# Kernel optimization log

Measured on AMD Instinct MI355X. Metric: run time of the kernel, lower is better.

## Reference

```python
import jax, jax.numpy as jnp
import numpy as np

B, D, H, L, E, NL, P, IMG, NT = 32, 768, 8, 6, 8, 256, 16, 224, 10
G = IMG // P          # 14 patches per side
NP = G * G            # 196 patches
HD = D // H           # 96 head dim
TOPK = 2
KEEP = 0.25
EPS = 1e-5


def layer_norm(x, g, b):
    m = x.mean(-1, keepdims=True)
    v = ((x - m) ** 2).mean(-1, keepdims=True)
    return (x - m) / jnp.sqrt(v + EPS) * g + b


def mha(q, kv, in_w, in_b, out_w, out_b):
    # torch nn.MultiheadAttention: packed in_proj (3D, D), out_proj (D, D)
    wq, wk, wv = in_w[:D], in_w[D:2 * D], in_w[2 * D:]
    bq, bk, bv = in_b[:D], in_b[D:2 * D], in_b[2 * D:]

    def heads(x, w, b):
        y = x @ w.T + b                               # (B, S, D)
        return y.reshape(x.shape[0], x.shape[1], H, HD).transpose(0, 2, 1, 3)

    Q = heads(q, wq, bq)
    K = heads(kv, wk, bk)
    V = heads(kv, wv, bv)
    scores = jnp.einsum('bhqd,bhkd->bhqk', Q, K) / np.sqrt(HD).astype(np.float32)
    attn = jax.nn.softmax(scores, axis=-1)
    o = jnp.einsum('bhqk,bhkd->bhqd', attn, V)
    o = o.transpose(0, 2, 1, 3).reshape(q.shape[0], q.shape[1], D)
    return o @ out_w.T + out_b


def moe(x, rw, rb, w1, b1, w2, b2):
    # top-2 routing; renormalize the top-k weights with a second softmax
    Bq, S, _ = x.shape
    T = Bq * S
    xt = x.reshape(T, D)
    probs = jax.nn.softmax(xt @ rw.T + rb, axis=-1)       # (T, E)
    tw, ti = jax.lax.top_k(probs, TOPK)                   # (T, K)
    tw = jax.nn.softmax(tw, axis=-1)
    # combine weights per expert: (T, E), >0 only for the chosen experts
    combine = (jax.nn.one_hot(ti, E, dtype=x.dtype) * tw[..., None]).sum(axis=1)
    out = jnp.zeros_like(xt)
    for e in range(E):  # fixed small expert count
        h = jax.nn.gelu(xt @ w1[e].T + b1[e], approximate=False)
        out = out + (h @ w2[e].T + b2[e]) * combine[:, e:e + 1]
    return out.reshape(Bq, S, D)


def _forward(images, type_ids, mask_noise, conv_w, conv_b, pos_emb, type_emb,
             latents, ca_in_w, ca_in_b, ca_out_w, ca_out_b, ca_ln_g, ca_ln_b,
             sa_in_w, sa_in_b, sa_out_w, sa_out_b, ln1_g, ln1_b,
             router_w, router_b, e_w1, e_b1, e_w2, e_b2, ln2_g, ln2_b):
    b = images.shape[0]
    # non-overlapping conv patch embed == unfold + matmul
    xp = images.reshape(b, 3, G, P, G, P).transpose(0, 2, 4, 1, 3, 5)
    xp = xp.reshape(b, NP, 3 * P * P)
    patches = xp @ conv_w.reshape(D, -1).T + conv_b        # (B, NP, D)
    patches = patches + pos_emb + type_emb[type_ids][:, None, :]
    # random masking: keep n_visible patches chosen by argsort of noise
    n_visible = int(NP * KEEP)
    order = jnp.argsort(mask_noise, axis=1)
    visible_indices = order[:, :n_visible]
    masked_indices = order[:, n_visible:]
    visible = jnp.take_along_axis(patches, visible_indices[:, :, None], axis=1)
    # cross attention from latents to visible patches
    lat = jnp.broadcast_to(latents, (b, NL, D))
    lat = layer_norm(lat + mha(lat, visible, ca_in_w, ca_in_b, ca_out_w, ca_out_b),
                     ca_ln_g, ca_ln_b)
    for l in range(L):
        a = mha(lat, lat, sa_in_w[l], sa_in_b[l], sa_out_w[l], sa_out_b[l])
        lat = layer_norm(lat + a, ln1_g[l], ln1_b[l])
        m = moe(lat, router_w[l], router_b[l], e_w1[l], e_b1[l], e_w2[l], e_b2[l])
        lat = layer_norm(lat + m, ln2_g[l], ln2_b[l])
    return lat, visible_indices, masked_indices


def setup_inputs() -> dict:
    key = jax.random.key(0)
    ks = jax.random.split(key, 16)
    r = lambda k, shape, s=0.02: jax.random.normal(k, shape, dtype=jnp.float32) * s
    z = lambda shape: jnp.zeros(shape, jnp.float32)
    o = lambda shape: jnp.ones(shape, jnp.float32)
    inp = {}
    inp['images'] = jax.random.normal(ks[0], (B, 3, IMG, IMG), dtype=jnp.float32)
    inp['type_ids'] = jax.random.randint(ks[1], (B,), 0, NT)
    inp['mask_noise'] = jax.random.uniform(ks[2], (B, NP), dtype=jnp.float32)
    inp['conv_w'] = r(ks[3], (D, 3, P, P))
    inp['conv_b'] = z((D,))
    inp['pos_emb'] = r(ks[4], (1, NP, D), 1.0)
    inp['type_emb'] = r(ks[5], (NT, D), 1.0)
    inp['latents'] = r(ks[6], (NL, D), 1.0)
    inp['ca_in_w'] = r(ks[7], (3 * D, D)); inp['ca_in_b'] = z((3 * D,))
    inp['ca_out_w'] = r(ks[8], (D, D)); inp['ca_out_b'] = z((D,))
    inp['ca_ln_g'] = o((D,)); inp['ca_ln_b'] = z((D,))
    inp['sa_in_w'] = r(ks[9], (L, 3 * D, D)); inp['sa_in_b'] = z((L, 3 * D))
    inp['sa_out_w'] = r(ks[10], (L, D, D)); inp['sa_out_b'] = z((L, D))
    inp['ln1_g'] = o((L, D)); inp['ln1_b'] = z((L, D))
    inp['router_w'] = r(ks[11], (L, E, D)); inp['router_b'] = z((L, E))
    inp['e_w1'] = r(ks[12], (L, E, 2 * D, D)); inp['e_b1'] = z((L, E, 2 * D))
    inp['e_w2'] = r(ks[13], (L, E, D, 2 * D)); inp['e_b2'] = z((L, E, D))
    inp['ln2_g'] = o((L, D)); inp['ln2_b'] = z((L, D))
    return inp


def reference(images, type_ids, mask_noise, conv_w, conv_b, pos_emb, type_emb,
              latents, ca_in_w, ca_in_b, ca_out_w, ca_out_b, ca_ln_g, ca_ln_b,
              sa_in_w, sa_in_b, sa_out_w, sa_out_b, ln1_g, ln1_b,
              router_w, router_b, e_w1, e_b1, e_w2, e_b2, ln2_g, ln2_b):
    return _forward(images, type_ids, mask_noise, conv_w, conv_b, pos_emb,
                    type_emb, latents, ca_in_w, ca_in_b, ca_out_w, ca_out_b,
                    ca_ln_g, ca_ln_b, sa_in_w, sa_in_b, sa_out_w, sa_out_b,
                    ln1_g, ln1_b, router_w, router_b, e_w1, e_b1, e_w2, e_b2,
                    ln2_g, ln2_b)
```

## Files before the change

### kernel.cpp

```cpp
#include <hip/hip_runtime.h>

typedef unsigned short u16;
typedef unsigned int u32;
typedef __attribute__((ext_vector_type(8))) u16 u16x8;
typedef __attribute__((ext_vector_type(8))) __bf16 bf16x8;
typedef __attribute__((ext_vector_type(4))) float f32x4;

#define DEV static __device__ __forceinline__

DEV float b2f(u16 u){ unsigned int i = ((unsigned int)u)<<16; float f; __builtin_memcpy(&f,&i,4); return f; }
DEV u16 f2b(float f){ unsigned int x; __builtin_memcpy(&x,&f,4); x = x + 0x7fffu + ((x>>16)&1u); return (u16)(x>>16); }

DEV void gll16(const u16* g, u16* l){
    __builtin_amdgcn_global_load_lds(
        (const __attribute__((address_space(1))) u32*)(const void*)g,
        (__attribute__((address_space(3))) u32*)(void*)l, 16, 0, 0);
}

template<bool F32>
DEV u16x8 ld8(const void* base, long off){
    if constexpr (F32){
        const float* p = (const float*)base + off;
        float4 a = *(const float4*)p;
        float4 b = *(const float4*)(p+4);
        u16x8 r;
        r[0]=f2b(a.x); r[1]=f2b(a.y); r[2]=f2b(a.z); r[3]=f2b(a.w);
        r[4]=f2b(b.x); r[5]=f2b(b.y); r[6]=f2b(b.z); r[7]=f2b(b.w);
        return r;
    } else {
        return *(const u16x8*)((const u16*)base + off);
    }
}
template<bool F32>
DEV const void* vadd(const void* p, long elems){
    if constexpr (F32) return (const void*)((const float*)p + elems);
    else               return (const void*)((const u16*)p + elems);
}

#define LAT_ELEMS 6291456
#define NVIS 49
#define NMASK 147
#define T_TOK 8192
#define MOE_CAP 17408
#define MOE_HALF 8704
#define KOFF 6291456L
#define VOFF 12582912L

__global__ __launch_bounds__(256) void wconv(const float* __restrict__ src, u16* __restrict__ dst, long n)
{
    long i = ((long)blockIdx.x*256 + threadIdx.x)*8;
    if (i >= n) return;
    *(u16x8*)(dst + i) = ld8<true>(src, i);
}

__global__ __launch_bounds__(256) void argsort_k(const float* __restrict__ noise,
                                                 int* __restrict__ order,
                                                 float* __restrict__ dout,
                                                 u16* __restrict__ zbuf)
{
    __shared__ float vals[196];
    __shared__ int ord[196];
    int b = blockIdx.x, tid = threadIdx.x;
    if (b == 0 && tid < 128) zbuf[tid] = 0;
    if (tid < 196) vals[tid] = noise[b*196 + tid];
    __syncthreads();
    if (tid < 196){
        float vi = vals[tid]; int rank = 0;
        for (int j=0;j<196;j++){ float vj = vals[j]; rank += (vj < vi) || (vj == vi && j < tid); }
        ord[rank] = tid;
    }
    __syncthreads();
    if (tid < 196){
        int v = ord[tid];
        order[b*196 + tid] = v;
        if (tid < NVIS) dout[LAT_ELEMS + b*NVIS + tid] = (float)v;
        else            dout[LAT_ELEMS + 32*NVIS + b*NMASK + (tid - NVIS)] = (float)v;
    }
}

__global__ __launch_bounds__(256) void patch_gather(const float* __restrict__ images,
                                                    const int* __restrict__ order,
                                                    u16* __restrict__ Ap)
{
    int i = blockIdx.x*256 + threadIdx.x;
    int t = i/48, kc = i - t*48;
    if (t >= 1664) return;
    if (t >= 1568){
        u16x8 z{};
        *(u16x8*)(Ap + (long)t*768 + kc*16)     = z;
        *(u16x8*)(Ap + (long)t*768 + kc*16 + 8) = z;
        return;
    }
    int b = t/49, vi = t - b*49;
    int p = order[b*196 + vi];
    int c = kc >> 4, py = kc & 15;
    int gy = p/14, gx = p - gy*14;
    const float* src = images + (((long)(b*3 + c)*224 + gy*16 + py)*224 + gx*16);
    u16x8 o0 = ld8<true>(src, 0);
    u16x8 o1 = ld8<true>(src, 8);
    *(u16x8*)(Ap + (long)t*768 + kc*16)     = o0;
    *(u16x8*)(Ap + (long)t*768 + kc*16 + 8) = o1;
}

__global__ __launch_bounds__(256) void add_pos_type(u16* __restrict__ vis,
                                                    const int* __restrict__ order,
                                                    const int* __restrict__ type_ids,
                                                    const float* __restrict__ pos,
                                                    const float* __restrict__ temb)
{
    int i = blockIdx.x*256 + threadIdx.x;
    int t = i/96, dc = (i - t*96)*8;
    if (t >= 1568) return;
    int b = t/49, vi = t - b*49;
    int p = order[b*196 + vi], tb = type_ids[b];
    u16x8 a = *(u16x8*)(vis + (long)t*768 + dc);
    const float* pp = pos  + (long)p*768 + dc;
    const float* tt = temb + (long)tb*768 + dc;
    float4 p0 = *(const float4*)pp, p1 = *(const float4*)(pp+4);
    float4 t0 = *(const float4*)tt, t1 = *(const float4*)(tt+4);
    u16x8 o;
    o[0]=f2b(b2f(a[0])+p0.x+t0.x); o[1]=f2b(b2f(a[1])+p0.y+t0.y);
    o[2]=f2b(b2f(a[2])+p0.z+t0.z); o[3]=f2b(b2f(a[3])+p0.w+t0.w);
    o[4]=f2b(b2f(a[4])+p1.x+t1.x); o[5]=f2b(b2f(a[5])+p1.y+t1.y);
    o[6]=f2b(b2f(a[6])+p1.z+t1.z); o[7]=f2b(b2f(a[7])+p1.w+t1.w);
    *(u16x8*)(vis + (long)t*768 + dc) = o;
}

template<int BK, bool BIAS, bool GELU, int GRP, bool AF32, bool BF32, bool SWZ, bool GLL>
__global__ __launch_bounds__(256,4) void gemm_nt(
    const void* __restrict__ A, const void* __restrict__ B, const float* __restrict__ bias,
    u16* __restrict__ C,
    int M, int N, int K, int lda, int ldb, int ldc,
    float scale, int ZLO, int NB,
    long sAh, long sAl, long sBh, long sBl, long sCh, long sCl,
    const int* __restrict__ aoff, const int* __restrict__ tos, const u16* __restrict__ zbuf,
    int row_base, long sBE, long sBiasE)
{
    int bx = blockIdx.x, by = blockIdx.y;
    if (SWZ){
        int nx = gridDim.x, ny = gridDim.y;
        int nwg = nx*ny;
        int flat = by*nx + bx;
        int q = nwg >> 3, r = nwg & 7;
        int xcd = flat & 7, idx = flat >> 3;
        int wg = (xcd < r ? xcd*(q+1) : r*(q+1) + (xcd - r)*q) + idx;
        bx = wg % nx; by = wg / nx;
    }
    int z = blockIdx.z; int zh = z / ZLO, zl = z - zh*ZLO;
    const void* Ab = vadd<AF32>(A, zh*sAh + zl*sAl);
    const void* Bb = vadd<BF32>(B, zh*sBh + zl*sBl);
    u16* Cb = C + zh*sCh + zl*sCl;
    const float* biasb = bias;
    int row0 = by*128, col0 = bx*128;
    int lim = 0;
    if (GRP == 1 || GRP == 2){
        lim = aoff[8];
        int g0 = row_base + row0;
        if (g0 >= lim) return;
        int e = 0;
        #pragma unroll
        for (int i=1;i<8;i++) if (g0 >= aoff[i]) e = i;
        Bb = vadd<BF32>(B, (long)e*sBE);
        if (BIAS) biasb = bias + (long)e*sBiasE;
    }
    constexpr int SP = GLL ? BK : BK + 8;
    __shared__ __align__(16) u16 As[128*SP];
    __shared__ __align__(16) u16 Bs[128*SP];
    int tid = threadIdx.x;
    int lane = tid & 63, wv = tid >> 6;
    int wr = (wv>>1)*64, wc = (wv&1)*64;
    f32x4 acc[4][4];
    #pragma unroll
    for (int m=0;m<4;m++){
        #pragma unroll
        for (int n=0;n<4;n++) acc[m][n] = f32x4{0.f,0.f,0.f,0.f};
    }
    constexpr int RPC = BK/8;
    constexpr int RPI = 64/RPC;
    constexpr int NJ  = 32/RPI;
    constexpr int PER = 128*RPC/256;
    int tA[4];
    if (GRP == 1){
        if (GLL){
            #pragma unroll
            for (int j=0;j<NJ;j++){
                int r = wv*32 + j*RPI + (lane/RPC);
                tA[j] = tos[row_base + row0 + r];
            }
        } else {
            #pragma unroll
            for (int j=0;j<PER && j<4;j++){
                int c = j*256 + tid;
                tA[j] = tos[row_base + row0 + c/RPC];
            }
        }
    }
    for (int k0=0; k0<K; k0+=BK){
        if constexpr (GLL){
            #pragma unroll
            for (int j=0;j<NJ;j++){
                int r  = wv*32 + j*RPI + (lane/RPC);
                int ch = lane % RPC;
                const u16* sa;
                if (GRP == 1){
                    int t = tA[j];
                    sa = (t >= 0) ? (const u16*)Ab + (long)t*lda + k0 + ch*8 : zbuf + ch*8;
                } else {
                    sa = (const u16*)Ab + (long)(row0+r)*lda + k0 + ch*8;
                }
                gll16(sa, As + (wv*32 + j*RPI)*BK);
                const u16* sb = (col0 + r < NB) ? (const u16*)Bb + (long)(col0+r)*ldb + k0 + ch*8
                                                : zbuf + ch*8;
                gll16(sb, Bs + (wv*32 + j*RPI)*BK);
            }
        } else {
            #pragma unroll
            for (int j=0;j<PER;j++){
                int c = j*256 + tid;
                int r = c / RPC, cc = (c - r*RPC)*8;
                u16x8 va{}, vb{};
                if (GRP == 1){
                    int t = tA[j];
                    if (t >= 0) va = ld8<AF32>(Ab, (long)t*lda + k0 + cc);
                } else {
                    va = ld8<AF32>(Ab, (long)(row0+r)*lda + k0 + cc);
                }
                if (col0 + r < NB) vb = ld8<BF32>(Bb, (long)(col0+r)*ldb + k0 + cc);
                *(u16x8*)(As + r*SP + cc) = va;
                *(u16x8*)(Bs + r*SP + cc) = vb;
            }
        }
        __syncthreads();
        #pragma unroll
        for (int kk=0; kk<BK/32; kk++){
            bf16x8 af[4], bg[4];
            #pragma unroll
            for (int m=0;m<4;m++)
                af[m] = *(const bf16x8*)(As + (wr + m*16 + (lane&15))*SP + kk*32 + (lane>>4)*8);
            #pragma unroll
            for (int n=0;n<4;n++)
                bg[n] = *(const bf16x8*)(Bs + (wc + n*16 + (lane&15))*SP + kk*32 + (lane>>4)*8);
            #pragma unroll
            for (int m=0;m<4;m++){
                #pragma unroll
                for (int n=0;n<4;n++)
                    acc[m][n] = __builtin_amdgcn_mfma_f32_16x16x32_bf16(af[m], bg[n], acc[m][n], 0,0,0);
            }
        }
        __syncthreads();
    }
    #pragma unroll
    for (int m=0;m<4;m++){
        int rbase = row0 + wr + m*16 + ((lane>>4)<<2);
        #pragma unroll
        for (int n=0;n<4;n++){
            int col = col0 + wc + n*16 + (lane&15);
            if (col < N){
                float bv = BIAS ? biasb[col] : 0.f;
                #pragma unroll
                for (int j=0;j<4;j++){
                    int row = rbase + j;
                    bool ok = (row < M);
                    if (GRP == 1 || GRP == 2) ok = ok && (row_base + row) < lim;
                    if (ok){
                        float v = acc[m][n][j]*scale + bv;
                        if (GELU) v = 0.5f*v*(1.f + erff(v*0.70710678118f));
                        u16 ov = f2b(v);
                        if (GRP == 3){
                            if (col < 768){
                                Cb[(long)row*768 + col] = ov;
                            } else if (col < 1536){
                                Cb[sBE + (long)row*768 + (col - 768)] = ov;
                            } else {
                                int c96 = col - 1536;
                                int h = c96/96, d = c96 - h*96;
                                Cb[sBiasE + ((long)((row>>8)*8 + h)*96 + d)*256 + (row & 255)] = ov;
                            }
                        } else if (GRP == 2){
                            Cb[(long)(row_base + row)*ldc + col] = ov;
                        } else {
                            Cb[(long)row*ldc + col] = ov;
                        }
                    }
                }
            }
        }
    }
}

__global__ __launch_bounds__(256,2) void scores_sm(const u16* __restrict__ Q,
                                                   const u16* __restrict__ K,
                                                   u16* __restrict__ S)
{
    __shared__ __align__(16) u16 As[128*32];
    __shared__ __align__(16) u16 Bs[256*32];
    int z = blockIdx.y;
    int b = z >> 3, h = z & 7;
    const u16* Ab = Q + (long)b*196608 + h*96 + (long)blockIdx.x*128*768;
    const u16* Bb = K + (long)b*196608 + h*96;
    int tid = threadIdx.x, lane = tid & 63, wv = tid >> 6;
    f32x4 acc[2][16];
    #pragma unroll
    for (int m=0;m<2;m++){
        #pragma unroll
        for (int n=0;n<16;n++) acc[m][n] = f32x4{0.f,0.f,0.f,0.f};
    }
    int ch = lane & 3, rr = lane >> 2;
    for (int k0=0;k0<96;k0+=32){
        #pragma unroll
        for (int j=0;j<2;j++){
            int r = wv*32 + j*16 + rr;
            gll16(Ab + (long)r*768 + k0 + ch*8, As + (wv*128 + j*64)*8);
        }
        #pragma unroll
        for (int j=0;j<4;j++){
            int r = wv*64 + j*16 + rr;
            gll16(Bb + (long)r*768 + k0 + ch*8, Bs + (wv*256 + j*64)*8);
        }
        __syncthreads();
        bf16x8 af[2];
        #pragma unroll
        for (int m=0;m<2;m++)
            af[m] = *(const bf16x8*)(As + (wv*32 + m*16 + (lane&15))*32 + (lane>>4)*8);
        #pragma unroll
        for (int n=0;n<16;n++){
            bf16x8 bg = *(const bf16x8*)(Bs + (n*16 + (lane&15))*32 + (lane>>4)*8);
            acc[0][n] = __builtin_amdgcn_mfma_f32_16x16x32_bf16(af[0], bg, acc[0][n], 0,0,0);
            acc[1][n] = __builtin_amdgcn_mfma_f32_16x16x32_bf16(af[1], bg, acc[1][n], 0,0,0);
        }
        __syncthreads();
    }
    const float SCL = 0.10206207f;
    u16* Sz = S + (long)z*65536 + (long)blockIdx.x*128*256;
    #pragma unroll
    for (int m=0;m<2;m++){
        #pragma unroll
        for (int j=0;j<4;j++){
            float mx = -1e30f;
            #pragma unroll
            for (int n=0;n<16;n++) mx = fmaxf(mx, acc[m][n][j]);
            #pragma unroll
            for (int off=8; off>=1; off>>=1) mx = fmaxf(mx, __shfl_xor(mx, off, 64));
            float ev[16]; float sum = 0.f;
            #pragma unroll
            for (int n=0;n<16;n++){ ev[n] = __expf((acc[m][n][j]-mx)*SCL); sum += ev[n]; }
            #pragma unroll
            for (int off=8; off>=1; off>>=1) sum += __shfl_xor(sum, off, 64);
            float inv = 1.f/sum;
            int row = wv*32 + m*16 + ((lane>>4)<<2) + j;
            #pragma unroll
            for (int n=0;n<16;n++) Sz[(long)row*256 + n*16 + (lane&15)] = f2b(ev[n]*inv);
        }
    }
}

__global__ __launch_bounds__(256) void ca_attn(const u16* __restrict__ Qc,
                                               const u16* __restrict__ KV,
                                               u16* __restrict__ attn_out)
{
    __shared__ float Sm[256*49];
    __shared__ u16 KVs[49*96];
    int b = blockIdx.x, h = blockIdx.y, q = threadIdx.x;
    for (int i=q; i<49*96; i+=256){ int k=i/96, d=i-k*96; KVs[i] = KV[(long)(b*49+k)*1536 + h*96 + d]; }
    __syncthreads();
    float qv[96];
    #pragma unroll
    for (int d=0;d<96;d++) qv[d] = b2f(Qc[(long)q*768 + h*96 + d]);
    for (int k=0;k<49;k++){
        float a = 0.f;
        #pragma unroll
        for (int d=0;d<96;d++) a += qv[d]*b2f(KVs[k*96+d]);
        Sm[q*49+k] = a*0.10206207f;
    }
    __syncthreads();
    for (int i=q; i<49*96; i+=256){ int k=i/96, d=i-k*96; KVs[i] = KV[(long)(b*49+k)*1536 + 768 + h*96 + d]; }
    float mx = -1e30f;
    for (int k=0;k<49;k++) mx = fmaxf(mx, Sm[q*49+k]);
    float sum = 0.f;
    for (int k=0;k<49;k++){ float e = __expf(Sm[q*49+k]-mx); Sm[q*49+k]=e; sum+=e; }
    float inv = 1.f/sum;
    __syncthreads();
    for (int d=0;d<96;d++){
        float a = 0.f;
        for (int k=0;k<49;k++) a += Sm[q*49+k]*b2f(KVs[k*96+d]);
        attn_out[(long)(b*256+q)*768 + h*96 + d] = f2b(a*inv);
    }
}

template<int MODE, bool ROUTE>
__global__ __launch_bounds__(256) void ln_k(
    const float* __restrict__ res, int resmod,
    const u16* __restrict__ add,
    const u16* __restrict__ OutE, const int* __restrict__ sot, const float2* __restrict__ w01,
    const float* __restrict__ g, const float* __restrict__ bb,
    const float* __restrict__ rw, const float* __restrict__ rb,
    int2* __restrict__ e01o, float2* __restrict__ w01o,
    float* __restrict__ out, u16* __restrict__ outb, int T)
{
    int wid = threadIdx.x >> 6, lane = threadIdx.x & 63;
    int t = blockIdx.x*4 + wid; if (t >= T) return;
    const float* rp = res + (long)(t % resmod)*768;
    float x[12];
    #pragma unroll
    for (int j=0;j<3;j++){
        float4 v = *(const float4*)(rp + j*256 + lane*4);
        x[j*4+0]=v.x; x[j*4+1]=v.y; x[j*4+2]=v.z; x[j*4+3]=v.w;
    }
    if (MODE == 0){
        const u16* ap = add + (long)t*768;
        #pragma unroll
        for (int j=0;j<3;j++){
            ushort4 v = *(const ushort4*)(ap + j*256 + lane*4);
            x[j*4+0]+=b2f(v.x); x[j*4+1]+=b2f(v.y); x[j*4+2]+=b2f(v.z); x[j*4+3]+=b2f(v.w);
        }
    } else {
        int s0 = sot[2*t], s1 = sot[2*t+1];
        float2 w = w01[t];
        const u16* p0 = OutE + (long)s0*768;
        const u16* p1 = OutE + (long)s1*768;
        #pragma unroll
        for (int j=0;j<3;j++){
            ushort4 v0 = *(const ushort4*)(p0 + j*256 + lane*4);
            ushort4 v1 = *(const ushort4*)(p1 + j*256 + lane*4);
            x[j*4+0] += w.x*b2f(v0.x) + w.y*b2f(v1.x);
            x[j*4+1] += w.x*b2f(v0.y) + w.y*b2f(v1.y);
            x[j*4+2] += w.x*b2f(v0.z) + w.y*b2f(v1.z);
            x[j*4+3] += w.x*b2f(v0.w) + w.y*b2f(v1.w);
        }
    }
    float s = 0.f;
    #pragma unroll
    for (int i=0;i<12;i++) s += x[i];
    #pragma unroll
    for (int off=32; off>=1; off>>=1) s += __shfl_xor(s, off, 64);
    float m = s*(1.f/768.f);
    float s2 = 0.f;
    #pragma unroll
    for (int i=0;i<12;i++){ float d = x[i]-m; s2 += d*d; }
    #pragma unroll
    for (int off=32; off>=1; off>>=1) s2 += __shfl_xor(s2, off, 64);
    float rstd = rsqrtf(s2*(1.f/768.f) + 1e-5f);
    float y[12];
    #pragma unroll
    for (int j=0;j<3;j++){
        int col = j*256 + lane*4;
        float4 gg = *(const float4*)(g + col);
        float4 bv = *(const float4*)(bb + col);
        y[j*4+0] = (x[j*4+0]-m)*rstd*gg.x + bv.x;
        y[j*4+1] = (x[j*4+1]-m)*rstd*gg.y + bv.y;
        y[j*4+2] = (x[j*4+2]-m)*rstd*gg.z + bv.z;
        y[j*4+3] = (x[j*4+3]-m)*rstd*gg.w + bv.w;
        float4 o; o.x=y[j*4+0]; o.y=y[j*4+1]; o.z=y[j*4+2]; o.w=y[j*4+3];
        *(float4*)(out + (long)t*768 + col) = o;
        if (outb != nullptr){
            ushort4 ob;
            ob.x = f2b(o.x); ob.y = f2b(o.y); ob.z = f2b(o.z); ob.w = f2b(o.w);
            *(ushort4*)(outb + (long)t*768 + col) = ob;
        }
    }
    if (ROUTE){
        float part[8];
        #pragma unroll
        for (int e=0;e<8;e++){
            const float* wp = rw + e*768;
            float a = 0.f;
            #pragma unroll
            for (int j=0;j<3;j++){
                float4 w4 = *(const float4*)(wp + j*256 + lane*4);
                a += y[j*4+0]*w4.x + y[j*4+1]*w4.y + y[j*4+2]*w4.z + y[j*4+3]*w4.w;
            }
            part[e] = a;
        }
        #pragma unroll
        for (int e=0;e<8;e++){
            #pragma unroll
            for (int off=32; off>=1; off>>=1) part[e] += __shfl_xor(part[e], off, 64);
        }
        if (lane == 0){
            float pe[8];
            float mx = -1e30f;
            #pragma unroll
            for (int e=0;e<8;e++){ pe[e] = part[e] + rb[e]; mx = fmaxf(mx, pe[e]); }
            float sum = 0.f;
            #pragma unroll
            for (int e=0;e<8;e++){ pe[e] = __expf(pe[e]-mx); sum += pe[e]; }
            float inv = 1.f/sum;
            #pragma unroll
            for (int e=0;e<8;e++) pe[e] *= inv;
            int i0 = 0;
            #pragma unroll
            for (int e=1;e<8;e++) if (pe[e] > pe[i0]) i0 = e;
            int i1 = -1;
            for (int e=0;e<8;e++){ if (e == i0) continue; if (i1 < 0 || pe[e] > pe[i1]) i1 = e; }
            float ex = __expf(pe[i1] - pe[i0]);
            float w0 = 1.f/(1.f+ex), w1 = ex/(1.f+ex);
            e01o[t] = int2{i0, i1};
            w01o[t] = float2{w0, w1};
        }
    }
}

__global__ __launch_bounds__(256) void route_build(const int2* __restrict__ e01,
                                                   int* __restrict__ aoff_g,
                                                   int* __restrict__ tos, int* __restrict__ sot,
                                                   u16* __restrict__ zbuf)
{
    __shared__ int wsum[8][4];
    __shared__ int wbase[8][4];
    __shared__ int aoff_s[9];
    int tid = threadIdx.x, lane = tid & 63, wid = tid >> 6;
    for (int s = tid; s < MOE_CAP; s += 256) tos[s] = -1;
    if (tid < 128) zbuf[tid] = 0;
    int t0 = tid * 32;
    int lc[8];
    #pragma unroll
    for (int e=0;e<8;e++) lc[e] = 0;
    for (int i=0;i<32;i++){
        int2 e = e01[t0+i];
        lc[e.x]++; lc[e.y]++;
    }
    int excl[8];
    #pragma unroll
    for (int e=0;e<8;e++){
        int sc = lc[e];
        #pragma unroll
        for (int off=1; off<64; off<<=1){
            int n = __shfl_up(sc, off, 64);
            if (lane >= off) sc += n;
        }
        excl[e] = sc - lc[e];
        if (lane == 63) wsum[e][wid] = sc;
    }
    __syncthreads();
    if (tid == 0){
        int tot = 0;
        #pragma unroll
        for (int e=0;e<8;e++){
            int s = 0;
            #pragma unroll
            for (int w=0;w<4;w++){ wbase[e][w] = s; s += wsum[e][w]; }
            aoff_s[e] = tot;
            tot += (s + 127) & ~127;
        }
        aoff_s[8] = tot;
        #pragma unroll
        for (int e=0;e<9;e++) aoff_g[e] = aoff_s[e];
    }
    __syncthreads();
    int cur[8];
    #pragma unroll
    for (int e=0;e<8;e++) cur[e] = aoff_s[e] + wbase[e][wid] + excl[e];
    for (int i=0;i<32;i++){
        int t = t0 + i;
        int2 e = e01[t];
        int s0 = cur[e.x]++;
        tos[s0] = t; sot[2*t]   = s0;
        int s1 = cur[e.y]++;
        tos[s1] = t; sot[2*t+1] = s1;
    }
}

extern "C" void kernel_launch(void* const* d_in, const int* in_sizes, int n_in,
                              void* d_out, int out_size, void* d_ws, size_t ws_size,
                              hipStream_t stream)
{
    (void)in_sizes; (void)n_in; (void)out_size;
    const float* images   = (const float*)d_in[0];
    const int*   type_ids = (const int*)d_in[1];
    const float* noise    = (const float*)d_in[2];
    const float* conv_w   = (const float*)d_in[3];
    const float* conv_b   = (const float*)d_in[4];
    const float* pos_emb  = (const float*)d_in[5];
    const float* type_emb = (const float*)d_in[6];
    const float* latents  = (const float*)d_in[7];
    const float* ca_in_w  = (const float*)d_in[8];
    const float* ca_in_b  = (const float*)d_in[9];
    const float* ca_out_w = (const float*)d_in[10];
    const float* ca_out_b = (const float*)d_in[11];
    const float* ca_ln_g  = (const float*)d_in[12];
    const float* ca_ln_b  = (const float*)d_in[13];
    const float* sa_in_w  = (const float*)d_in[14];
    const float* sa_in_b  = (const float*)d_in[15];
    const float* sa_out_w = (const float*)d_in[16];
    const float* sa_out_b = (const float*)d_in[17];
    const float* ln1_g    = (const float*)d_in[18];
    const float* ln1_b    = (const float*)d_in[19];
    const float* router_w = (const float*)d_in[20];
    const float* router_b = (const float*)d_in[21];
    const float* e_w1     = (const float*)d_in[22];
    const float* e_b1     = (const float*)d_in[23];
    const float* e_w2     = (const float*)d_in[24];
    const float* e_b2     = (const float*)d_in[25];
    const float* ln2_g    = (const float*)d_in[26];
    const float* ln2_b    = (const float*)d_in[27];
    float* dout = (float*)d_out;
    float* lat  = dout;

    char* p = (char*)d_ws;
    auto alloc = [&](size_t n)->char*{ char* r = p; p += (n + 255) & ~(size_t)255; return r; };
    int*    order  = (int*)   alloc(32*196*4);
    int2*   e01    = (int2*)  alloc((size_t)T_TOK*8);
    float2* w01    = (float2*)alloc((size_t)T_TOK*8);
    int*    aoff   = (int*)   alloc(64);
    int*    tos    = (int*)   alloc((size_t)MOE_CAP*4);
    int*    sot    = (int*)   alloc((size_t)T_TOK*2*4);
    u16*    zbuf   = (u16*)   alloc(256);
    size_t aux_used = (size_t)(p - (char*)d_ws);
    const size_t WB_BYTES = 92798976ull + 260702208ull;
    bool wb  = ws_size >= aux_used + WB_BYTES;
    bool big = wb || ws_size >= aux_used + 92798976ull;
    u16* ar = (u16*)alloc(wb ? WB_BYTES : (big ? 92798976ull : 71303168ull));
    u16* latb   = big ? ar : nullptr;
    u16* common = big ? ar + 6291456 : ar;
    u16* wbufA  = wb ? ar + 6291456 + 40108032 : nullptr;
    u16* Ap  = common;
    u16* vis = common + 1277952;
    u16* KV  = common + 2555904;
    u16* Qc  = common + 5111808;
    u16* caO = common + 5308416;
    u16* caM = common + 11599872;
    u16* Qb  = common;
    u16* Vt  = common + VOFF;
    u16* S   = common + 18874368;
    u16* aO  = common;
    u16* mha = common + KOFF;
    u16* Hbuf = common;
    u16* OutE = common + (big ? 26738688 : 13369344);
    u16* cwb      = wbufA;
    u16* cainb    = wbufA + 589824;
    u16* caoutb   = wbufA + 2359296;
    u16* winbAll  = wbufA + 2949120;
    u16* woutbAll = wbufA + 13565952;
    u16* w1bAll   = wbufA + 17104896;
    u16* w2bAll   = wbufA + 73728000;

    const float ONE = 1.0f;
    const long Z0 = 0;

    argsort_k<<<32, 256, 0, stream>>>(noise, order, dout, zbuf);
    patch_gather<<<312, 256, 0, stream>>>(images, order, Ap);
    if (wb){
        wconv<<<288, 256, 0, stream>>>(conv_w, cwb, 589824);
        wconv<<<864, 256, 0, stream>>>(ca_in_w, cainb, 1769472);
        wconv<<<288, 256, 0, stream>>>(ca_out_w, caoutb, 589824);
        wconv<<<5184, 256, 0, stream>>>(sa_in_w, winbAll, 10616832);
        wconv<<<1728, 256, 0, stream>>>(sa_out_w, woutbAll, 3538944);
        wconv<<<27648, 256, 0, stream>>>(e_w1, w1bAll, 56623104);
        wconv<<<27648, 256, 0, stream>>>(e_w2, w2bAll, 56623104);
        gemm_nt<64,true,false,0,false,false,true,true><<<dim3(6,13,1),256,0,stream>>>(Ap, cwb, conv_b, vis,
            1664,768,768, 768,768,768, ONE, 1, 768, Z0,Z0,Z0,Z0,Z0,Z0, nullptr,nullptr,zbuf,0, Z0,Z0);
        add_pos_type<<<588, 256, 0, stream>>>(vis, order, type_ids, pos_emb, type_emb);
        gemm_nt<64,true,false,0,true,false,true,false><<<dim3(6,2,1),256,0,stream>>>(latents, cainb, ca_in_b, Qc,
            256,768,768, 768,768,768, ONE, 1, 768, Z0,Z0,Z0,Z0,Z0,Z0, nullptr,nullptr,zbuf,0, Z0,Z0);
        gemm_nt<64,true,false,0,false,false,true,true><<<dim3(12,13,1),256,0,stream>>>(vis, cainb + 589824, ca_in_b + 768, KV,
            1664,1536,768, 768,768,1536, ONE, 1, 1536, Z0,Z0,Z0,Z0,Z0,Z0, nullptr,nullptr,zbuf,0, Z0,Z0);
        ca_attn<<<dim3(32,8), 256, 0, stream>>>(Qc, KV, caO);
        gemm_nt<64,true,false,0,false,false,true,true><<<dim3(6,64,1),256,0,stream>>>(caO, caoutb, ca_out_b, caM,
            T_TOK,768,768, 768,768,768, ONE, 1, 768, Z0,Z0,Z0,Z0,Z0,Z0, nullptr,nullptr,zbuf,0, Z0,Z0);
    } else {
        gemm_nt<64,true,false,0,false,true,false,false><<<dim3(6,13,1),256,0,stream>>>(Ap, conv_w, conv_b, vis,
            1664,768,768, 768,768,768, ONE, 1, 768, Z0,Z0,Z0,Z0,Z0,Z0, nullptr,nullptr,zbuf,0, Z0,Z0);
        add_pos_type<<<588, 256, 0, stream>>>(vis, order, type_ids, pos_emb, type_emb);
        gemm_nt<64,true,false,0,true,true,false,false><<<dim3(6,2,1),256,0,stream>>>(latents, ca_in_w, ca_in_b, Qc,
            256,768,768, 768,768,768, ONE, 1, 768, Z0,Z0,Z0,Z0,Z0,Z0, nullptr,nullptr,zbuf,0, Z0,Z0);
        gemm_nt<64,true,false,0,false,true,false,false><<<dim3(12,13,1),256,0,stream>>>(vis, ca_in_w + 768*768, ca_in_b + 768, KV,
            1664,1536,768, 768,768,1536, ONE, 1, 1536, Z0,Z0,Z0,Z0,Z0,Z0, nullptr,nullptr,zbuf,0, Z0,Z0);
        ca_attn<<<dim3(32,8), 256, 0, stream>>>(Qc, KV, caO);
        gemm_nt<64,true,false,0,false,true,false,false><<<dim3(6,64,1),256,0,stream>>>(caO, ca_out_w, ca_out_b, caM,
            T_TOK,768,768, 768,768,768, ONE, 1, 768, Z0,Z0,Z0,Z0,Z0,Z0, nullptr,nullptr,zbuf,0, Z0,Z0);
    }
    ln_k<0,false><<<2048, 256, 0, stream>>>(latents, 256, caM, nullptr,nullptr,nullptr, ca_ln_g, ca_ln_b,
        nullptr,nullptr,nullptr,nullptr, lat, latb, T_TOK);

    for (int l=0; l<6; l++){
        const float* b_in  = sa_in_b  + l*2304;
        const float* b_out = sa_out_b + l*768;
        const float* b1 = e_b1 + l*8*1536;
        const float* b2 = e_b2 + l*8*768;
        const float* rwl = router_w + l*8*768;
        const float* rbl = router_b + l*8;
        if (wb){
            const u16* winb  = winbAll  + (long)l*1769472;
            const u16* woutb = woutbAll + (long)l*589824;
            const u16* w1b   = w1bAll   + (long)l*9437184;
            const u16* w2b   = w2bAll   + (long)l*9437184;
            gemm_nt<64,true,false,3,false,false,true,true><<<dim3(18,64,1),256,0,stream>>>(latb, winb, b_in, Qb,
                T_TOK,2304,768, 768,768,0, ONE, 1, 2304, Z0,Z0,Z0,Z0,Z0,Z0, nullptr,nullptr,zbuf,0, KOFF, VOFF);
            scores_sm<<<dim3(2,256), 256, 0, stream>>>(Qb, Qb + KOFF, S);
            gemm_nt<64,false,false,0,false,false,false,true><<<dim3(1,2,256),256,0,stream>>>(S, Vt, nullptr, aO,
                256,96,256, 256,256,768, ONE, 8, 96, 524288,65536, 196608,24576, 196608,96, nullptr,nullptr,zbuf,0, Z0,Z0);
            gemm_nt<64,true,false,0,false,false,true,true><<<dim3(6,64,1),256,0,stream>>>(aO, woutb, b_out, mha,
                T_TOK,768,768, 768,768,768, ONE, 1, 768, Z0,Z0,Z0,Z0,Z0,Z0, nullptr,nullptr,zbuf,0, Z0,Z0);
            ln_k<0,true><<<2048, 256, 0, stream>>>(lat, T_TOK, mha, nullptr,nullptr,nullptr, ln1_g + l*768, ln1_b + l*768,
                rwl, rbl, e01, w01, lat, latb, T_TOK);
            route_build<<<1, 256, 0, stream>>>(e01, aoff, tos, sot, zbuf);
            gemm_nt<64,true,true,1,false,false,true,true><<<dim3(12,136,1),256,0,stream>>>(latb, w1b, b1, Hbuf,
                MOE_CAP,1536,768, 768,768,1536, ONE, 1, 1536, Z0,Z0,Z0,Z0,Z0,Z0,
                aoff, tos, zbuf, 0, (long)1536*768, 1536);
            gemm_nt<64,true,false,2,false,false,true,true><<<dim3(6,136,1),256,0,stream>>>(Hbuf, w2b, b2, OutE,
                MOE_CAP,768,1536, 1536,1536,768, ONE, 1, 768, Z0,Z0,Z0,Z0,Z0,Z0,
                aoff, tos, zbuf, 0, (long)768*1536, 768);
            ln_k<1,false><<<2048, 256, 0, stream>>>(lat, T_TOK, nullptr, OutE, sot, w01, ln2_g + l*768, ln2_b + l*768,
                nullptr,nullptr,nullptr,nullptr, lat, latb, T_TOK);
        } else {
            const float* w_in  = sa_in_w  + (long)l*2304*768;
            const float* w_out = sa_out_w + (long)l*768*768;
            const float* w1 = e_w1 + (long)l*8*1536*768;
            const float* w2 = e_w2 + (long)l*8*768*1536;
            if (big){
                gemm_nt<64,true,false,3,false,true,false,false><<<dim3(18,64,1),256,0,stream>>>(latb, w_in, b_in, Qb,
                    T_TOK,2304,768, 768,768,0, ONE, 1, 2304, Z0,Z0,Z0,Z0,Z0,Z0, nullptr,nullptr,zbuf,0, KOFF, VOFF);
            } else {
                gemm_nt<64,true,false,3,true,true,false,false><<<dim3(18,64,1),256,0,stream>>>(lat, w_in, b_in, Qb,
                    T_TOK,2304,768, 768,768,0, ONE, 1, 2304, Z0,Z0,Z0,Z0,Z0,Z0, nullptr,nullptr,zbuf,0, KOFF, VOFF);
            }
            scores_sm<<<dim3(2,256), 256, 0, stream>>>(Qb, Qb + KOFF, S);
            gemm_nt<64,false,false,0,false,false,false,true><<<dim3(1,2,256),256,0,stream>>>(S, Vt, nullptr, aO,
                256,96,256, 256,256,768, ONE, 8, 96, 524288,65536, 196608,24576, 196608,96, nullptr,nullptr,zbuf,0, Z0,Z0);
            gemm_nt<64,true,false,0,false,true,false,false><<<dim3(6,64,1),256,0,stream>>>(aO, w_out, b_out, mha,
                T_TOK,768,768, 768,768,768, ONE, 1, 768, Z0,Z0,Z0,Z0,Z0,Z0, nullptr,nullptr,zbuf,0, Z0,Z0);
            ln_k<0,true><<<2048, 256, 0, stream>>>(lat, T_TOK, mha, nullptr,nullptr,nullptr, ln1_g + l*768, ln1_b + l*768,
                rwl, rbl, e01, w01, lat, latb, T_TOK);
            route_build<<<1, 256, 0, stream>>>(e01, aoff, tos, sot, zbuf);
            if (big){
                gemm_nt<64,true,true,1,false,true,false,false><<<dim3(12,136,1),256,0,stream>>>(latb, w1, b1, Hbuf,
                    MOE_CAP,1536,768, 768,768,1536, ONE, 1, 1536, Z0,Z0,Z0,Z0,Z0,Z0,
                    aoff, tos, zbuf, 0, (long)1536*768, 1536);
                gemm_nt<64,true,false,2,false,true,false,false><<<dim3(6,136,1),256,0,stream>>>(Hbuf, w2, b2, OutE,
                    MOE_CAP,768,1536, 1536,1536,768, ONE, 1, 768, Z0,Z0,Z0,Z0,Z0,Z0,
                    aoff, tos, zbuf, 0, (long)768*1536, 768);
            } else {
                for (int rb2=0; rb2<MOE_CAP; rb2+=MOE_HALF){
                    gemm_nt<64,true,true,1,true,true,false,false><<<dim3(12,68,1),256,0,stream>>>(lat, w1, b1, Hbuf,
                        MOE_HALF,1536,768, 768,768,1536, ONE, 1, 1536, Z0,Z0,Z0,Z0,Z0,Z0,
                        aoff, tos, zbuf, rb2, (long)1536*768, 1536);
                    gemm_nt<64,true,false,2,false,true,false,false><<<dim3(6,68,1),256,0,stream>>>(Hbuf, w2, b2, OutE,
                        MOE_HALF,768,1536, 1536,1536,768, ONE, 1, 768, Z0,Z0,Z0,Z0,Z0,Z0,
                        aoff, tos, zbuf, rb2, (long)768*1536, 768);
                }
            }
            ln_k<1,false><<<2048, 256, 0, stream>>>(lat, T_TOK, nullptr, OutE, sot, w01, ln2_g + l*768, ln2_b + l*768,
                nullptr,nullptr,nullptr,nullptr, lat, latb, T_TOK);
        }
    }
}
```

Measured before the change: 2.407 ms.

## Fuse self-attention scores, softmax and PV product into one kernel

```diff
diff --git a/kernel.cpp b/kernel.cpp
--- a/kernel.cpp
+++ b/kernel.cpp
@@ -288,68 +288,79 @@
     }
 }
 
-__global__ __launch_bounds__(256,2) void scores_sm(const u16* __restrict__ Q,
-                                                   const u16* __restrict__ K,
-                                                   u16* __restrict__ S)
-{
-    __shared__ __align__(16) u16 As[128*32];
-    __shared__ __align__(16) u16 Bs[256*32];
+__global__ __launch_bounds__(256,3) void attn_fused(const u16* __restrict__ Q,
+                                                    const u16* __restrict__ K,
+                                                    const u16* __restrict__ Vt,
+                                                    u16* __restrict__ aO)
+{
+    __shared__ __align__(16) u16 sm[16896];
+    u16* As = sm;
+    u16* Bs = sm + 2048;
+    u16* Pl = sm;
     int z = blockIdx.y;
     int b = z >> 3, h = z & 7;
-    const u16* Ab = Q + (long)b*196608 + h*96 + (long)blockIdx.x*128*768;
-    const u16* Bb = K + (long)b*196608 + h*96;
+    int q0 = blockIdx.x * 64;
+    const u16* Ab = Q  + (long)b*196608 + h*96 + (long)q0*768;
+    const u16* Bb = K  + (long)b*196608 + h*96;
+    const u16* Vz = Vt + (long)z*24576;
     int tid = threadIdx.x, lane = tid & 63, wv = tid >> 6;
-    f32x4 acc[2][16];
-    #pragma unroll
-    for (int m=0;m<2;m++){
-        #pragma unroll
-        for (int n=0;n<16;n++) acc[m][n] = f32x4{0.f,0.f,0.f,0.f};
-    }
     int ch = lane & 3, rr = lane >> 2;
+    f32x4 acc[16];
+    #pragma unroll
+    for (int n=0;n<16;n++) acc[n] = f32x4{0.f,0.f,0.f,0.f};
     for (int k0=0;k0<96;k0+=32){
-        #pragma unroll
-        for (int j=0;j<2;j++){
-            int r = wv*32 + j*16 + rr;
-            gll16(Ab + (long)r*768 + k0 + ch*8, As + (wv*128 + j*64)*8);
-        }
-        #pragma unroll
-        for (int j=0;j<4;j++){
-            int r = wv*64 + j*16 + rr;
-            gll16(Bb + (long)r*768 + k0 + ch*8, Bs + (wv*256 + j*64)*8);
-        }
+        gll16(Ab + (long)(wv*16 + rr)*768 + k0 + ch*8, As + (wv*16)*32);
+        #pragma unroll
+        for (int jj=0;jj<4;jj++)
+            gll16(Bb + (long)(wv*64 + jj*16 + rr)*768 + k0 + ch*8, Bs + (wv*64 + jj*16)*32);
         __syncthreads();
-        bf16x8 af[2];
-        #pragma unroll
-        for (int m=0;m<2;m++)
-            af[m] = *(const bf16x8*)(As + (wv*32 + m*16 + (lane&15))*32 + (lane>>4)*8);
+        bf16x8 af = *(const bf16x8*)(As + (wv*16 + (lane&15))*32 + (lane>>4)*8);
         #pragma unroll
         for (int n=0;n<16;n++){
             bf16x8 bg = *(const bf16x8*)(Bs + (n*16 + (lane&15))*32 + (lane>>4)*8);
-            acc[0][n] = __builtin_amdgcn_mfma_f32_16x16x32_bf16(af[0], bg, acc[0][n], 0,0,0);
-            acc[1][n] = __builtin_amdgcn_mfma_f32_16x16x32_bf16(af[1], bg, acc[1][n], 0,0,0);
+            acc[n] = __builtin_amdgcn_mfma_f32_16x16x32_bf16(af, bg, acc[n], 0,0,0);
         }
         __syncthreads();
     }
     const float SCL = 0.10206207f;
-    u16* Sz = S + (long)z*65536 + (long)blockIdx.x*128*256;
-    #pragma unroll
-    for (int m=0;m<2;m++){
+    #pragma unroll
+    for (int j=0;j<4;j++){
+        float mx = -1e30f;
+        #pragma unroll
+        for (int n=0;n<16;n++) mx = fmaxf(mx, acc[n][j]);
+        #pragma unroll
+        for (int off=8; off>=1; off>>=1) mx = fmaxf(mx, __shfl_xor(mx, off, 64));
+        float ev[16]; float sum = 0.f;
+        #pragma unroll
+        for (int n=0;n<16;n++){ ev[n] = __expf((acc[n][j]-mx)*SCL); sum += ev[n]; }
+        #pragma unroll
+        for (int off=8; off>=1; off>>=1) sum += __shfl_xor(sum, off, 64);
+        float inv = 1.f/sum;
+        int row = wv*16 + ((lane>>4)<<2) + j;
+        #pragma unroll
+        for (int n=0;n<16;n++) Pl[row*264 + n*16 + (lane&15)] = f2b(ev[n]*inv);
+    }
+    __syncthreads();
+    f32x4 acc2[6];
+    #pragma unroll
+    for (int dn=0;dn<6;dn++) acc2[dn] = f32x4{0.f,0.f,0.f,0.f};
+    #pragma unroll
+    for (int kk=0;kk<8;kk++){
+        bf16x8 pa = *(const bf16x8*)(Pl + (wv*16 + (lane&15))*264 + kk*32 + (lane>>4)*8);
+        #pragma unroll
+        for (int dn=0;dn<6;dn++){
+            bf16x8 bg = *(const bf16x8*)(Vz + (long)(dn*16 + (lane&15))*256 + kk*32 + (lane>>4)*8);
+            acc2[dn] = __builtin_amdgcn_mfma_f32_16x16x32_bf16(pa, bg, acc2[dn], 0,0,0);
+        }
+    }
+    u16* outp = aO + (long)b*196608 + h*96 + (long)q0*768;
+    #pragma unroll
+    for (int dn=0;dn<6;dn++){
+        int d = dn*16 + (lane&15);
         #pragma unroll
         for (int j=0;j<4;j++){
-            float mx = -1e30f;
-            #pragma unroll
-            for (int n=0;n<16;n++) mx = fmaxf(mx, acc[m][n][j]);
-            #pragma unroll
-            for (int off=8; off>=1; off>>=1) mx = fmaxf(mx, __shfl_xor(mx, off, 64));
-            float ev[16]; float sum = 0.f;
-            #pragma unroll
-            for (int n=0;n<16;n++){ ev[n] = __expf((acc[m][n][j]-mx)*SCL); sum += ev[n]; }
-            #pragma unroll
-            for (int off=8; off>=1; off>>=1) sum += __shfl_xor(sum, off, 64);
-            float inv = 1.f/sum;
-            int row = wv*32 + m*16 + ((lane>>4)<<2) + j;
-            #pragma unroll
-            for (int n=0;n<16;n++) Sz[(long)row*256 + n*16 + (lane&15)] = f2b(ev[n]*inv);
+            int row = wv*16 + ((lane>>4)<<2) + j;
+            outp[(long)row*768 + d] = f2b(acc2[dn][j]);
         }
     }
 }
@@ -621,7 +632,6 @@
     u16* caM = common + 11599872;
     u16* Qb  = common;
     u16* Vt  = common + VOFF;
-    u16* S   = common + 18874368;
     u16* aO  = common;
     u16* mha = common + KOFF;
     u16* Hbuf = common;
@@ -686,9 +696,7 @@
             const u16* w2b   = w2bAll   + (long)l*9437184;
             gemm_nt<64,true,false,3,false,false,true,true><<<dim3(18,64,1),256,0,stream>>>(latb, winb, b_in, Qb,
                 T_TOK,2304,768, 768,768,0, ONE, 1, 2304, Z0,Z0,Z0,Z0,Z0,Z0, nullptr,nullptr,zbuf,0, KOFF, VOFF);
-            scores_sm<<<dim3(2,256), 256, 0, stream>>>(Qb, Qb + KOFF, S);
-            gemm_nt<64,false,false,0,false,false,false,true><<<dim3(1,2,256),256,0,stream>>>(S, Vt, nullptr, aO,
-                256,96,256, 256,256,768, ONE, 8, 96, 524288,65536, 196608,24576, 196608,96, nullptr,nullptr,zbuf,0, Z0,Z0);
+            attn_fused<<<dim3(4,256), 256, 0, stream>>>(Qb, Qb + KOFF, Vt, aO);
             gemm_nt<64,true,false,0,false,false,true,true><<<dim3(6,64,1),256,0,stream>>>(aO, woutb, b_out, mha,
                 T_TOK,768,768, 768,768,768, ONE, 1, 768, Z0,Z0,Z0,Z0,Z0,Z0, nullptr,nullptr,zbuf,0, Z0,Z0);
             ln_k<0,true><<<2048, 256, 0, stream>>>(lat, T_TOK, mha, nullptr,nullptr,nullptr, ln1_g + l*768, ln1_b + l*768,
@@ -714,9 +722,7 @@
                 gemm_nt<64,true,false,3,true,true,false,false><<<dim3(18,64,1),256,0,stream>>>(lat, w_in, b_in, Qb,
                     T_TOK,2304,768, 768,768,0, ONE, 1, 2304, Z0,Z0,Z0,Z0,Z0,Z0, nullptr,nullptr,zbuf,0, KOFF, VOFF);
             }
-            scores_sm<<<dim3(2,256), 256, 0, stream>>>(Qb, Qb + KOFF, S);
-            gemm_nt<64,false,false,0,false,false,false,true><<<dim3(1,2,256),256,0,stream>>>(S, Vt, nullptr, aO,
-                256,96,256, 256,256,768, ONE, 8, 96, 524288,65536, 196608,24576, 196608,96, nullptr,nullptr,zbuf,0, Z0,Z0);
+            attn_fused<<<dim3(4,256), 256, 0, stream>>>(Qb, Qb + KOFF, Vt, aO);
             gemm_nt<64,true,false,0,false,true,false,false><<<dim3(6,64,1),256,0,stream>>>(aO, w_out, b_out, mha,
                 T_TOK,768,768, 768,768,768, ONE, 1, 768, Z0,Z0,Z0,Z0,Z0,Z0, nullptr,nullptr,zbuf,0, Z0,Z0);
             ln_k<0,true><<<2048, 256, 0, stream>>>(lat, T_TOK, mha, nullptr,nullptr,nullptr, ln1_g + l*768, ln1_b + l*768,
```

Result: no change. 2.436 ms (+1.2%).
